# Performance work log

Measured on AMD Instinct MI355X. Metric: run time of the kernel, lower is better.

The kernel has to match this reference:

```python
import jax, jax.numpy as jnp
import numpy as np

K1, K2, ALPHA = 0.01, 0.03, 0.84
SIGMA_LEVELS = (1, 2, 4, 7)

def _box_conv(x, k):
    # x: [B,1,H,W]; uniform k x k mean filter, padding k//2 (matches F.conv2d)
    p = k // 2
    w = jnp.ones((1, 1, k, k), x.dtype) / (k * k)
    return jax.lax.conv_general_dilated(
        x, w, window_strides=(1, 1), padding=((p, p), (p, p)),
        dimension_numbers=('NCHW', 'OIHW', 'NCHW'))

def _ssim_mean(X, Y, C1, C2, k):
    ux = _box_conv(X, k)
    uy = _box_conv(Y, k)
    uxx = _box_conv(X * X, k)
    uyy = _box_conv(Y * Y, k)
    uxy = _box_conv(X * Y, k)
    vx = uxx - ux * ux
    vy = uyy - uy * uy
    vxy = uxy - ux * uy
    A1 = 2 * ux * uy + C1
    A2 = 2 * vxy + C2
    B1 = ux * ux + uy * uy + C1
    B2 = vx + vy + C2
    S = (A1 * A2) / (B1 * B2)
    return jnp.mean(S)

def setup_inputs() -> dict:
    key = jax.random.key(0)
    k1, k2 = jax.random.split(key)
    B, H, W = 128, 384, 384
    X = jax.random.uniform(k1, (B, H, W), dtype=jnp.float32)
    Y = jax.random.uniform(k2, (B, H, W), dtype=jnp.float32)
    data_range = jnp.ones((B,), dtype=jnp.float32)
    return {"X": X, "Y": Y, "data_range": data_range}

def reference(X, Y, data_range):
    X4 = X[:, None, :, :]   # [B,1,H,W]
    Y4 = Y[:, None, :, :]
    dr = data_range[:, None, None, None]  # [B,1,1,1]
    C1 = (K1 * dr) ** 2
    C2 = (K2 * dr) ** 2
    # msssim = product of scalar SSIM means over sigma levels (ones_like * scalars).mean()
    msssim = jnp.float32(1.0)
    for k in SIGMA_LEVELS:
        msssim = msssim * _ssim_mean(X4, Y4, C1, C2, k)
    msssim_loss = 1.0 - msssim
    kM = SIGMA_LEVELS[-1]
    fX = _box_conv(X4, kM)
    fY = _box_conv(Y4, kM)
    l1 = jnp.mean(jnp.abs(fX - fY))
    return ALPHA * msssim_loss + (1.0 - ALPHA) * l1
```

## Files before the change

### kernel.cpp

```cpp
#include <hip/hip_runtime.h>


#define W 384
#define H 384
#define NB 128
#define BAND 48
#define NTILES 7
#define NBLK (NTILES * 2 * NB)

__device__ __forceinline__ float bp(int addr, float v) {
    return __int_as_float(__builtin_amdgcn_ds_bpermute(addr, __float_as_int(v)));
}

__device__ __forceinline__ float ssim_u(const float* V, float k2, float c1k4, float c2k4) {
    const float Sx = V[0], Sy = V[1], Sxx = V[2], Syy = V[3], Sxy = V[4];
    const float p  = Sx * Sy;
    float sq = Sx * Sx;
    sq = fmaf(Sy, Sy, sq);
    const float A1 = fmaf(2.f, p, c1k4);
    const float t  = fmaf(k2, Sxy, -p);
    const float A2 = fmaf(2.f, t, c2k4);
    const float B1 = sq + c1k4;
    const float sw = Sxx + Syy;
    const float B2 = fmaf(k2, sw, -sq) + c2k4;
    return (A1 * A2) * __builtin_amdgcn_rcpf(B1 * B2);
}

__global__ __launch_bounds__(256) void msssim_main(
    const float* __restrict__ X, const float* __restrict__ Y,
    const float* __restrict__ dr, float* __restrict__ part)
{
    const int lane = threadIdx.x & 63;
    const int wv   = threadIdx.x >> 6;
    const int tile = blockIdx.x;
    const int band = blockIdx.y * 4 + wv;
    const int b    = blockIdx.z;

    const int cbase = -3 + 56 * tile;
    const int c     = cbase + lane;
    const int R0    = BAND * band;

    const int g1hi  = R0 + 48;
    const int g24hi = (band == 7) ? 385 : R0 + 48;

    const float drb = dr[b];
    const float C1 = (0.01f * drb) * (0.01f * drb);
    const float C2 = (0.03f * drb) * (0.03f * drb);
    const float C1_2 = C1 * 16.f,   C2_2 = C2 * 16.f;
    const float C1_4 = C1 * 256.f,  C2_4 = C2 * 256.f;
    const float C1_7 = C1 * 2401.f, C2_7 = C2 * 2401.f;

    const float m1 = (lane >= 3 && lane <= 58 && c     <= 383) ? 1.f : 0.f;
    const float m2 = (lane >= 2 && lane <= 57 && c + 1 <= 384) ? 1.f : 0.f;
    const float m4 = (lane >= 1 && lane <= 56 && c + 2 <= 384) ? 1.f : 0.f;
    const float m7 = (             lane <= 55 && c + 3 <= 383) ? 1.f : 0.f;

    const float mcol = (c >= 0 && c < W) ? 1.f : 0.f;
    const int   cc   = c < 0 ? 0 : (c > W - 1 ? W - 1 : c);

    int ad[6];
#pragma unroll
    for (int d = 1; d <= 6; ++d) ad[d - 1] = ((lane + d) & 63) << 2;

    const float* __restrict__ Xb = X + (size_t)b * (H * W);
    const float* __restrict__ Yb = Y + (size_t)b * (H * W);

    float r2[5], r4[3][5], r7[6][5];
#pragma unroll
    for (int q = 0; q < 5; ++q) {
        r2[q] = 0.f;
        r4[0][q] = r4[1][q] = r4[2][q] = 0.f;
#pragma unroll
        for (int a = 0; a < 6; ++a) r7[a][q] = 0.f;
    }

    float ss1 = 0.f, ss2 = 0.f, ss4 = 0.f, ss7 = 0.f, l1 = 0.f;

    const int u0 = R0 - 3;

    float px[6], py[6];
    auto loadv = [&](int u, float& x, float& y) {
        if (u >= 0 && u < H) {
            x = Xb[(size_t)u * W + cc];
            y = Yb[(size_t)u * W + cc];
        } else { x = 0.f; y = 0.f; }
    };

    float Ax[7], Ay[7], Bx[7], By[7];
    auto do_bperm = [&](float xr, float yr, float* sx, float* sy) {
        const float xv = xr * mcol;
        const float yv = yr * mcol;
        sx[0] = xv; sy[0] = yv;
#pragma unroll
        for (int d = 1; d <= 6; ++d) {
            sx[d] = bp(ad[d - 1], xv);
            sy[d] = bp(ad[d - 1], yv);
        }
    };

    loadv(u0,     px[0], py[0]);
    loadv(u0 + 1, px[1], py[1]);
    loadv(u0 + 2, px[2], py[2]);
    do_bperm(px[0], py[0], Ax, Ay);

    for (int s = 0; s < 54; s += 6) {
#pragma unroll
        for (int ph = 0; ph < 6; ++ph) {
            const int u = u0 + s + ph;

            loadv(u + 3, px[(ph + 3) % 6], py[(ph + 3) % 6]);

            const bool evenT = ((ph & 1) == 0);
            float* nx = evenT ? Bx : Ax;
            float* ny = evenT ? By : Ay;
            const float* xa = evenT ? Ax : Bx;
            const float* ya = evenT ? Ay : By;
            do_bperm(px[(ph + 1) % 6], py[(ph + 1) % 6], nx, ny);

            float V2[5], V4[5], V7[5];
#pragma unroll
            for (int q = 0; q < 5; ++q) {
                float e[7];
#pragma unroll
                for (int i = 0; i < 7; ++i) {
                    e[i] = (q == 0) ? xa[i]
                         : (q == 1) ? ya[i]
                         : (q == 2) ? xa[i] * xa[i]
                         : (q == 3) ? ya[i] * ya[i]
                         :            xa[i] * ya[i];
                }
                const float w2 = e[0] + e[1];
                const float w4 = w2 + (e[2] + e[3]);
                const float w7 = w4 + ((e[4] + e[5]) + e[6]);
                V2[q] = w2 + r2[q];
                V4[q] = w4 + (r4[0][q] + r4[1][q] + r4[2][q]);
                V7[q] = w7 + ((r7[0][q] + r7[1][q]) + (r7[2][q] + r7[3][q])
                              + (r7[4][q] + r7[5][q]));
                r2[q] = w2;
                r4[2][q] = r4[1][q]; r4[1][q] = r4[0][q]; r4[0][q] = w4;
                r7[5][q] = r7[4][q]; r7[4][q] = r7[3][q]; r7[3][q] = r7[2][q];
                r7[2][q] = r7[1][q]; r7[1][q] = r7[0][q]; r7[0][q] = w7;
            }

            if (u >= R0 && u < g1hi) {
                const float xv = xa[0], yv = ya[0];
                const float s1 = fmaf(2.f, xv * yv, C1) *
                                 __builtin_amdgcn_rcpf(fmaf(xv, xv, fmaf(yv, yv, C1)));
                ss1 = fmaf(s1, m1, ss1);
            }
            if (u >= R0 && u < g24hi) {
                ss2 = fmaf(ssim_u(V2, 4.f, C1_2, C2_2), m2, ss2);
            }
            {
                const int i = u - 1;
                if (i >= R0 && i < g24hi) {
                    ss4 = fmaf(ssim_u(V4, 16.f, C1_4, C2_4), m4, ss4);
                }
            }
            {
                const int i = u - 3;
                if (i >= R0 && i < g1hi) {
                    ss7 = fmaf(ssim_u(V7, 49.f, C1_7, C2_7), m7, ss7);
                    l1  = fmaf(fabsf(V7[0] - V7[1]), m7, l1);
                }
            }
        }
    }

#pragma unroll
    for (int d = 32; d > 0; d >>= 1) {
        ss1 += __shfl_down(ss1, d, 64);
        ss2 += __shfl_down(ss2, d, 64);
        ss4 += __shfl_down(ss4, d, 64);
        ss7 += __shfl_down(ss7, d, 64);
        l1  += __shfl_down(l1,  d, 64);
    }
    __shared__ float sred[4][5];
    if (lane == 0) {
        sred[wv][0] = ss1; sred[wv][1] = ss2; sred[wv][2] = ss4;
        sred[wv][3] = ss7; sred[wv][4] = l1;
    }
    __syncthreads();
    if (threadIdx.x == 0) {
        const int bid = ((int)blockIdx.z * 2 + (int)blockIdx.y) * NTILES + (int)blockIdx.x;
#pragma unroll
        for (int q = 0; q < 5; ++q)
            part[bid * 5 + q] = sred[0][q] + sred[1][q] + sred[2][q] + sred[3][q];
    }
}

__global__ __launch_bounds__(256) void reduce_final(
    const float* __restrict__ part, float* __restrict__ out)
{
    const int lane = threadIdx.x & 63;
    const int wv   = threadIdx.x >> 6;
    double d[5] = {0, 0, 0, 0, 0};
    for (int i = threadIdx.x; i < NBLK; i += 256) {
#pragma unroll
        for (int q = 0; q < 5; ++q) d[q] += (double)part[i * 5 + q];
    }
#pragma unroll
    for (int s = 32; s > 0; s >>= 1) {
#pragma unroll
        for (int q = 0; q < 5; ++q) d[q] += __shfl_down(d[q], s, 64);
    }
    __shared__ double sd[4][5];
    if (lane == 0) {
#pragma unroll
        for (int q = 0; q < 5; ++q) sd[wv][q] = d[q];
    }
    __syncthreads();
    if (threadIdx.x == 0) {
        double a[5];
#pragma unroll
        for (int q = 0; q < 5; ++q)
            a[q] = sd[0][q] + sd[1][q] + sd[2][q] + sd[3][q];
        const double n384 = (double)NB * 384.0 * 384.0;
        const double n385 = (double)NB * 385.0 * 385.0;
        const double m  = (a[0] / n384) * (a[1] / n385) * (a[2] / n385) * (a[3] / n384);
        const double l1 = a[4] / 49.0 / n384;
        out[0] = (float)(0.84 * (1.0 - m) + 0.16 * l1);
    }
}

extern "C" void kernel_launch(void* const* d_in, const int* in_sizes, int n_in,
                              void* d_out, int out_size, void* d_ws, size_t ws_size,
                              hipStream_t stream) {
    const float* X  = (const float*)d_in[0];
    const float* Y  = (const float*)d_in[1];
    const float* dr = (const float*)d_in[2];
    float* out  = (float*)d_out;
    float* part = (float*)d_ws;

    dim3 grid(NTILES, 2, NB);
    msssim_main<<<grid, 256, 0, stream>>>(X, Y, dr, part);
    reduce_final<<<1, 256, 0, stream>>>(part, out);
}
```

Measured before the change: 229.2 us.

## Use sum/difference basis and prefix-doubling shuffles with running vertical sums

Rewrites the SSIM statistics in terms of p=x+y and m=x-y. This cuts the channels from five (x,y,xx,yy,xy) to four (p,m,pp,mm), since the cross term falls out of pp-mm. Horizontal window sums now come from a doubling scheme that needs four bpermutes per channel instead of six. Vertical 4- and 7-row sums use running accumulators instead of re-adding ring buffers. Constants are rescaled to match, and the extra rounding from the running sums and cancellation may shift accuracy slightly.

```diff
diff --git a/kernel.cpp b/kernel.cpp
--- a/kernel.cpp
+++ b/kernel.cpp
@@ -12,17 +12,17 @@
     return __int_as_float(__builtin_amdgcn_ds_bpermute(addr, __float_as_int(v)));
 }
 
-__device__ __forceinline__ float ssim_u(const float* V, float k2, float c1k4, float c2k4) {
-    const float Sx = V[0], Sy = V[1], Sxx = V[2], Syy = V[3], Sxy = V[4];
-    const float p  = Sx * Sy;
-    float sq = Sx * Sx;
-    sq = fmaf(Sy, Sy, sq);
-    const float A1 = fmaf(2.f, p, c1k4);
-    const float t  = fmaf(k2, Sxy, -p);
-    const float A2 = fmaf(2.f, t, c2k4);
-    const float B1 = sq + c1k4;
-    const float sw = Sxx + Syy;
-    const float B2 = fmaf(k2, sw, -sq) + c2k4;
+__device__ __forceinline__ float ssim_pm(const float* V, float k2, float c1k42, float c2k42) {
+    const float p2 = V[0] * V[0];
+    const float m2 = V[1] * V[1];
+    const float d  = p2 - m2;
+    const float s  = p2 + m2;
+    const float dq = V[2] - V[3];
+    const float sq = V[2] + V[3];
+    const float A1 = d + c1k42;
+    const float B1 = s + c1k42;
+    const float A2 = fmaf(k2, dq, -d) + c2k42;
+    const float B2 = fmaf(k2, sq, -s) + c2k42;
     return (A1 * A2) * __builtin_amdgcn_rcpf(B1 * B2);
 }
 
@@ -46,9 +46,10 @@
     const float drb = dr[b];
     const float C1 = (0.01f * drb) * (0.01f * drb);
     const float C2 = (0.03f * drb) * (0.03f * drb);
-    const float C1_2 = C1 * 16.f,   C2_2 = C2 * 16.f;
-    const float C1_4 = C1 * 256.f,  C2_4 = C2 * 256.f;
-    const float C1_7 = C1 * 2401.f, C2_7 = C2 * 2401.f;
+    const float tC1 = 2.f * C1;
+    const float C1_2 = C1 * 32.f,    C2_2 = C2 * 32.f;
+    const float C1_4 = C1 * 512.f,   C2_4 = C2 * 512.f;
+    const float C1_7 = C1 * 4802.f,  C2_7 = C2 * 4802.f;
 
     const float m1 = (lane >= 3 && lane <= 58 && c     <= 383) ? 1.f : 0.f;
     const float m2 = (lane >= 2 && lane <= 57 && c + 1 <= 384) ? 1.f : 0.f;
@@ -58,20 +59,22 @@
     const float mcol = (c >= 0 && c < W) ? 1.f : 0.f;
     const int   cc   = c < 0 ? 0 : (c > W - 1 ? W - 1 : c);
 
-    int ad[6];
-#pragma unroll
-    for (int d = 1; d <= 6; ++d) ad[d - 1] = ((lane + d) & 63) << 2;
+    const int a1 = ((lane + 1) & 63) << 2;
+    const int a2 = ((lane + 2) & 63) << 2;
+    const int a4 = ((lane + 4) & 63) << 2;
+    const int a6 = ((lane + 6) & 63) << 2;
 
     const float* __restrict__ Xb = X + (size_t)b * (H * W);
     const float* __restrict__ Yb = Y + (size_t)b * (H * W);
 
-    float r2[5], r4[3][5], r7[6][5];
-#pragma unroll
-    for (int q = 0; q < 5; ++q) {
+    float r2[4], r4[3][4], r7[6][4], v4s[4], v7s[4];
+#pragma unroll
+    for (int q = 0; q < 4; ++q) {
         r2[q] = 0.f;
         r4[0][q] = r4[1][q] = r4[2][q] = 0.f;
 #pragma unroll
         for (int a = 0; a < 6; ++a) r7[a][q] = 0.f;
+        v4s[q] = 0.f; v7s[q] = 0.f;
     }
 
     float ss1 = 0.f, ss2 = 0.f, ss4 = 0.f, ss7 = 0.f, l1 = 0.f;
@@ -86,22 +89,33 @@
         } else { x = 0.f; y = 0.f; }
     };
 
-    float Ax[7], Ay[7], Bx[7], By[7];
-    auto do_bperm = [&](float xr, float yr, float* sx, float* sy) {
-        const float xv = xr * mcol;
-        const float yv = yr * mcol;
-        sx[0] = xv; sy[0] = yv;
-#pragma unroll
-        for (int d = 1; d <= 6; ++d) {
-            sx[d] = bp(ad[d - 1], xv);
-            sy[d] = bp(ad[d - 1], yv);
+    float SA[14], SB[14];
+    auto stage = [&](float xr, float yr, float* S) {
+        const float pv  = (xr + yr) * mcol;
+        const float mv  = (xr - yr) * mcol;
+        const float ppv = pv * pv;
+        const float mmv = mv * mv;
+        S[12] = ppv; S[13] = mmv;
+        const float qv[4] = { pv, mv, ppv, mmv };
+#pragma unroll
+        for (int q = 0; q < 4; ++q) {
+            const float v   = qv[q];
+            const float sh1 = bp(a1, v);
+            const float t   = v + sh1;
+            const float sh2 = bp(a2, t);
+            const float sh4 = bp(a4, t);
+            const float sh6 = bp(a6, v);
+            const float w4  = t + sh2;
+            S[q]     = t;
+            S[4 + q] = w4;
+            S[8 + q] = w4 + (sh4 + sh6);
         }
     };
 
     loadv(u0,     px[0], py[0]);
     loadv(u0 + 1, px[1], py[1]);
     loadv(u0 + 2, px[2], py[2]);
-    do_bperm(px[0], py[0], Ax, Ay);
+    stage(px[0], py[0], SA);
 
     for (int s = 0; s < 54; s += 6) {
 #pragma unroll
@@ -111,57 +125,43 @@
             loadv(u + 3, px[(ph + 3) % 6], py[(ph + 3) % 6]);
 
             const bool evenT = ((ph & 1) == 0);
-            float* nx = evenT ? Bx : Ax;
-            float* ny = evenT ? By : Ay;
-            const float* xa = evenT ? Ax : Bx;
-            const float* ya = evenT ? Ay : By;
-            do_bperm(px[(ph + 1) % 6], py[(ph + 1) % 6], nx, ny);
-
-            float V2[5], V4[5], V7[5];
-#pragma unroll
-            for (int q = 0; q < 5; ++q) {
-                float e[7];
-#pragma unroll
-                for (int i = 0; i < 7; ++i) {
-                    e[i] = (q == 0) ? xa[i]
-                         : (q == 1) ? ya[i]
-                         : (q == 2) ? xa[i] * xa[i]
-                         : (q == 3) ? ya[i] * ya[i]
-                         :            xa[i] * ya[i];
-                }
-                const float w2 = e[0] + e[1];
-                const float w4 = w2 + (e[2] + e[3]);
-                const float w7 = w4 + ((e[4] + e[5]) + e[6]);
-                V2[q] = w2 + r2[q];
-                V4[q] = w4 + (r4[0][q] + r4[1][q] + r4[2][q]);
-                V7[q] = w7 + ((r7[0][q] + r7[1][q]) + (r7[2][q] + r7[3][q])
-                              + (r7[4][q] + r7[5][q]));
-                r2[q] = w2;
-                r4[2][q] = r4[1][q]; r4[1][q] = r4[0][q]; r4[0][q] = w4;
+            float* Sn       = evenT ? SB : SA;
+            const float* Sv = evenT ? SA : SB;
+            stage(px[(ph + 1) % 6], py[(ph + 1) % 6], Sn);
+
+            float V2[4], V4[4], V7[4];
+#pragma unroll
+            for (int q = 0; q < 4; ++q) {
+                const float w2v = Sv[q], w4v = Sv[4 + q], w7v = Sv[8 + q];
+                V2[q] = w2v + r2[q];  r2[q] = w2v;
+                const float a4v = w4v + v4s[q];
+                V4[q] = a4v;  v4s[q] = a4v - r4[2][q];
+                r4[2][q] = r4[1][q]; r4[1][q] = r4[0][q]; r4[0][q] = w4v;
+                const float a7v = w7v + v7s[q];
+                V7[q] = a7v;  v7s[q] = a7v - r7[5][q];
                 r7[5][q] = r7[4][q]; r7[4][q] = r7[3][q]; r7[3][q] = r7[2][q];
-                r7[2][q] = r7[1][q]; r7[1][q] = r7[0][q]; r7[0][q] = w7;
+                r7[2][q] = r7[1][q]; r7[1][q] = r7[0][q]; r7[0][q] = w7v;
             }
 
             if (u >= R0 && u < g1hi) {
-                const float xv = xa[0], yv = ya[0];
-                const float s1 = fmaf(2.f, xv * yv, C1) *
-                                 __builtin_amdgcn_rcpf(fmaf(xv, xv, fmaf(yv, yv, C1)));
-                ss1 = fmaf(s1, m1, ss1);
+                const float num = (Sv[12] - Sv[13]) + tC1;
+                const float den = (Sv[12] + Sv[13]) + tC1;
+                ss1 = fmaf(num * __builtin_amdgcn_rcpf(den), m1, ss1);
             }
             if (u >= R0 && u < g24hi) {
-                ss2 = fmaf(ssim_u(V2, 4.f, C1_2, C2_2), m2, ss2);
+                ss2 = fmaf(ssim_pm(V2, 4.f, C1_2, C2_2), m2, ss2);
             }
             {
                 const int i = u - 1;
                 if (i >= R0 && i < g24hi) {
-                    ss4 = fmaf(ssim_u(V4, 16.f, C1_4, C2_4), m4, ss4);
+                    ss4 = fmaf(ssim_pm(V4, 16.f, C1_4, C2_4), m4, ss4);
                 }
             }
             {
                 const int i = u - 3;
                 if (i >= R0 && i < g1hi) {
-                    ss7 = fmaf(ssim_u(V7, 49.f, C1_7, C2_7), m7, ss7);
-                    l1  = fmaf(fabsf(V7[0] - V7[1]), m7, l1);
+                    ss7 = fmaf(ssim_pm(V7, 49.f, C1_7, C2_7), m7, ss7);
+                    l1  = fmaf(fabsf(V7[1]), m7, l1);
                 }
             }
         }
```

Measured after the change: 223.1 us. 2.6% less time.
